# Kernel optimization log

Hardware: AMD Instinct MI355X
Metric: run time of the kernel (lower is better)

Reference implementation:

```python
import jax, jax.numpy as jnp
import numpy as np

DIM = 2048
N_HEADS = 16
HEAD_DIM = DIM // N_HEADS
ROPE_DIMS = 16
SEQ_LEN = 512
BATCH = 16


def _rope_cache(T):
    # freqs: [T, rd/2]
    inv = 1.0 / (10000.0 ** (jnp.arange(0, ROPE_DIMS, 2, dtype=jnp.float32) / ROPE_DIMS))
    t = jnp.arange(T, dtype=jnp.float32)
    freqs = jnp.outer(t, inv)
    return jnp.cos(freqs), jnp.sin(freqs)


def _apply_rope(x, cos, sin):
    # x: [B, H, T, hd]; rotate first ROPE_DIMS dims (half-split style)
    rd = ROPE_DIMS
    x_rope, x_pass = x[..., :rd], x[..., rd:]
    x1, x2 = x_rope[..., : rd // 2], x_rope[..., rd // 2:]
    c = cos[None, None, :, :]
    s = sin[None, None, :, :]
    rot = jnp.concatenate([x1 * c - x2 * s, x2 * c + x1 * s], axis=-1)
    return jnp.concatenate([rot, x_pass], axis=-1)


def setup_inputs() -> dict:
    key = jax.random.key(0)
    k1, k2, k3 = jax.random.split(key, 3)
    x = jax.random.normal(k1, (BATCH, SEQ_LEN, DIM), dtype=jnp.float32)
    Wqkv = jax.random.normal(k2, (DIM, 3 * DIM), dtype=jnp.float32) * (1.0 / np.sqrt(DIM))
    Wout = jax.random.normal(k3, (DIM, DIM), dtype=jnp.float32) * (1.0 / np.sqrt(DIM))
    return {"x": x, "Wqkv": Wqkv, "Wout": Wout}


def reference(x, Wqkv, Wout):
    B, T, C = x.shape
    H, hd = N_HEADS, HEAD_DIM
    qkv = (x @ Wqkv).reshape(B, T, 3, H, hd)
    q, k, v = qkv[:, :, 0], qkv[:, :, 1], qkv[:, :, 2]  # [B, T, H, hd]
    q = jnp.transpose(q, (0, 2, 1, 3))  # [B, H, T, hd]
    k = jnp.transpose(k, (0, 2, 1, 3))
    v = jnp.transpose(v, (0, 2, 1, 3))
    cos, sin = _rope_cache(T)
    q = _apply_rope(q, cos, sin)
    k = _apply_rope(k, cos, sin)
    scale = 1.0 / np.sqrt(hd)
    scores = jnp.einsum('bhqd,bhkd->bhqk', q, k) * scale
    causal = jnp.tril(jnp.ones((T, T), dtype=bool))
    scores = jnp.where(causal[None, None], scores, jnp.finfo(scores.dtype).min)
    attn = jax.nn.softmax(scores, axis=-1)
    y = jnp.einsum('bhqk,bhkd->bhqd', attn, v)  # [B, H, T, hd]
    y = jnp.transpose(y, (0, 2, 1, 3)).reshape(B, T, C)
    return y @ Wout
```

## Files before the change

### kernel.cpp

```cpp
#include <hip/hip_runtime.h>
#include <hip/hip_bf16.h>
#include <math.h>

using bf16 = __hip_bfloat16;
typedef short s16x8 __attribute__((ext_vector_type(8)));
typedef short s16x4 __attribute__((ext_vector_type(4)));
typedef float f32x4 __attribute__((ext_vector_type(4)));

#define DIM_C   2048
#define NHEADS  16
#define HEADD   128
#define SEQT    512
#define NBATCH  16
#define MROWS   (NBATCH*SEQT)
#define QKVN    (3*DIM_C)

static __device__ __forceinline__ float bf2f(bf16 v){ return __bfloat162float(v); }

static __device__ __forceinline__ void gl16(const void* g, void* l){
    __builtin_amdgcn_global_load_lds(
        reinterpret_cast<__attribute__((address_space(1))) void*>(
            (unsigned long long)g),
        reinterpret_cast<__attribute__((address_space(3))) void*>(
            (unsigned long long)l),
        16, 0, 0);
}

__global__ void k_cvt(const float* __restrict__ in, bf16* __restrict__ out, int n){
    size_t i = ((size_t)blockIdx.x*blockDim.x + threadIdx.x)*8;
    if (i >= (size_t)n) return;
    float4 a = *(const float4*)(in+i);
    float4 b = *(const float4*)(in+i+4);
    union { bf16 o[8]; s16x8 v; } u;
    u.o[0]=__float2bfloat16(a.x); u.o[1]=__float2bfloat16(a.y);
    u.o[2]=__float2bfloat16(a.z); u.o[3]=__float2bfloat16(a.w);
    u.o[4]=__float2bfloat16(b.x); u.o[5]=__float2bfloat16(b.y);
    u.o[6]=__float2bfloat16(b.z); u.o[7]=__float2bfloat16(b.w);
    *(s16x8*)(out+i) = u.v;
}

__global__ void k_transpose_cvt(const float* __restrict__ in, bf16* __restrict__ out,
                                int R, int C){
    __shared__ float tile[32][33];
    int c0 = blockIdx.x*32, r0 = blockIdx.y*32;
    int tx = threadIdx.x, ty = threadIdx.y;
    #pragma unroll
    for(int i=0;i<4;i++)
        tile[ty+8*i][tx] = in[(size_t)(r0+ty+8*i)*C + c0+tx];
    __syncthreads();
    #pragma unroll
    for(int i=0;i<4;i++)
        out[(size_t)(c0+ty+8*i)*R + r0+tx] = __float2bfloat16(tile[tx][ty+8*i]);
}

__global__ void k_vtrans(const bf16* __restrict__ qkv, bf16* __restrict__ vt){
    __shared__ bf16 tile[32][33];
    int t0 = blockIdx.x*32, d0 = blockIdx.y*32, bh = blockIdx.z;
    int b = bh>>4, h = bh&15;
    int tx = threadIdx.x, ty = threadIdx.y;
    const bf16* src = qkv + ((size_t)b*SEQT)*QKVN + 2*DIM_C + (size_t)h*HEADD;
    #pragma unroll
    for(int i=0;i<4;i++)
        tile[ty+8*i][tx] = src[(size_t)(t0+ty+8*i)*QKVN + d0+tx];
    __syncthreads();
    bf16* dst = vt + ((size_t)bh*HEADD)*SEQT;
    #pragma unroll
    for(int i=0;i<4;i++)
        dst[(size_t)(d0+ty+8*i)*SEQT + t0+tx] = tile[tx][ty+8*i];
}

__global__ void k_rope(bf16* __restrict__ qkv){
    int tid = blockIdx.x*blockDim.x + threadIdx.x;
    int i   = tid & 7;        int rest = tid >> 3;
    int qk  = rest & 1;       rest >>= 1;
    int h   = rest & 15;      rest >>= 4;
    int t   = rest & 511;     int b = rest >> 9;
    size_t base = ((size_t)(b*SEQT + t))*QKVN + (size_t)qk*DIM_C + (size_t)h*HEADD;
    float x1 = bf2f(qkv[base+i]), x2 = bf2f(qkv[base+i+8]);
    float inv = powf(10000.f, -(float)i/8.f);
    float fr = (float)t * inv;
    float c = cosf(fr), s = sinf(fr);
    qkv[base+i]   = __float2bfloat16(x1*c - x2*s);
    qkv[base+i+8] = __float2bfloat16(x2*c + x1*s);
}

static __device__ __forceinline__ void store_c(bf16* p, float v){ *p = __float2bfloat16(v); }
static __device__ __forceinline__ void store_c(float* p, float v){ *p = v; }

#define BAR()   __builtin_amdgcn_s_barrier()
#define SCHED() __builtin_amdgcn_sched_barrier(0)
#define LGKM0() asm volatile("s_waitcnt lgkmcnt(0)" ::: "memory")
#define VM6()   asm volatile("s_waitcnt vmcnt(6)"   ::: "memory")
#define VM0()   asm volatile("s_waitcnt vmcnt(0)"   ::: "memory")

template<typename OutT>
__global__ __launch_bounds__(512, 2) void k_gemm256(const bf16* __restrict__ A,
                                                    const bf16* __restrict__ Bt,
                                                    OutT* __restrict__ C,
                                                    int M, int N, int K){
    __shared__ __align__(16) bf16 AS[2][2][128*64];
    __shared__ __align__(16) bf16 BS[2][2][128*64];
    const int tid = threadIdx.x;
    const int wave = tid>>6, lane = tid&63, quad = lane>>4, l16 = lane&15;
    const int wm = wave>>2, wn = wave&3;

    const int nbx = gridDim.x;
    const int nwg = gridDim.x*gridDim.y;
    int bid = blockIdx.y*nbx + blockIdx.x;
    int swz = (bid&7)*(nwg>>3) + (bid>>3);
    int by = swz / nbx, bx = swz - by*nbx;
    const size_t rowbase = (size_t)by * 256;
    const size_t colbase = (size_t)bx * 256;
    const int NT = K>>6;

    f32x4 acc[8][4];
    #pragma unroll
    for(int i=0;i<8;i++)
        #pragma unroll
        for(int j=0;j<4;j++) acc[i][j] = (f32x4)(0.f);

    int cb0 = wave*64,        cc0 = cb0 + lane;
    int cb1 = 512 + wave*64,  cc1 = cb1 + lane;
    int ri0 = cc0>>3, gg0 = (cc0&7)^(ri0&7);
    int ri1 = cc1>>3, gg1 = (cc1&7)^(ri1&7);
    const bf16* pA0[2];  const bf16* pA1[2];
    const bf16* pB0[2];  const bf16* pB1[2];
    pA0[0] = A  + (rowbase + (size_t)(((ri0>>6)<<7) + (ri0&63)))*(size_t)K + gg0*8;
    pA0[1] = A  + (rowbase + (size_t)(((ri1>>6)<<7) + (ri1&63)))*(size_t)K + gg1*8;
    pA1[0] = pA0[0] + (size_t)64*K;  pA1[1] = pA0[1] + (size_t)64*K;
    pB0[0] = Bt + (colbase + (size_t)(((ri0>>5)<<6) + (ri0&31)))*(size_t)K + gg0*8;
    pB0[1] = Bt + (colbase + (size_t)(((ri1>>5)<<6) + (ri1&31)))*(size_t)K + gg1*8;
    pB1[0] = pB0[0] + (size_t)32*K;  pB1[1] = pB0[1] + (size_t)32*K;
    const int dE0 = cb0*8, dE1 = cb1*8;

    const int x7 = l16 & 7;
    int aB[2], bB[2];
    #pragma unroll
    for(int kc=0;kc<2;kc++){
        int ch = ((kc*4+quad) ^ x7) << 3;
        aB[kc] = (wm*64 + l16)*64 + ch;
        bB[kc] = (wn*32 + l16)*64 + ch;
    }

    s16x8 af[4][2], bf0[2][2], bf1[2][2];

#define READ_AF(BUF,MH) do{ _Pragma("unroll")                                    \
    for(int kc_=0;kc_<2;kc_++){ _Pragma("unroll")                                \
        for(int mi_=0;mi_<4;mi_++)                                               \
            af[mi_][kc_] = *(const s16x8*)(&AS[BUF][MH][aB[kc_] + mi_*1024]); } }while(0)
#define READ_BF(BUF,NH,DST) do{ _Pragma("unroll")                                \
    for(int kc_=0;kc_<2;kc_++){ _Pragma("unroll")                                \
        for(int nj_=0;nj_<2;nj_++)                                               \
            DST[nj_][kc_] = *(const s16x8*)(&BS[BUF][NH][bB[kc_] + nj_*1024]); } }while(0)
#define MFMA16(BFR,MH,NH) do{ _Pragma("unroll")                                  \
    for(int kc_=0;kc_<2;kc_++){ _Pragma("unroll")                                \
        for(int mi_=0;mi_<4;mi_++){ _Pragma("unroll")                            \
            for(int nj_=0;nj_<2;nj_++)                                           \
                acc[(MH)*4+mi_][(NH)*2+nj_] =                                    \
                    __builtin_amdgcn_mfma_f32_16x16x32_bf16(                     \
                        af[mi_][kc_], BFR[nj_][kc_],                             \
                        acc[(MH)*4+mi_][(NH)*2+nj_], 0,0,0); } } }while(0)

#define STG_A0(BUF,OFF) do{ gl16(pA0[0]+(OFF), &AS[BUF][0][dE0]);                \
                            gl16(pA0[1]+(OFF), &AS[BUF][0][dE1]); }while(0)
#define STG_A1(BUF,OFF) do{ gl16(pA1[0]+(OFF), &AS[BUF][1][dE0]);                \
                            gl16(pA1[1]+(OFF), &AS[BUF][1][dE1]); }while(0)
#define STG_B0(BUF,OFF) do{ gl16(pB0[0]+(OFF), &BS[BUF][0][dE0]);                \
                            gl16(pB0[1]+(OFF), &BS[BUF][0][dE1]); }while(0)
#define STG_B1(BUF,OFF) do{ gl16(pB1[0]+(OFF), &BS[BUF][1][dE0]);                \
                            gl16(pB1[1]+(OFF), &BS[BUF][1][dE1]); }while(0)

#define TILE(BUF,O1,O2,GA1,GR)                                                   \
    do{                                                                          \
                                                                         \
        if (GA1) STG_A1(BUF^1, O1);                                              \
        READ_AF(BUF,0); READ_BF(BUF,0,bf0);                                      \
        BAR(); LGKM0(); SCHED();                                                 \
        __builtin_amdgcn_s_setprio(1);  MFMA16(bf0,0,0);                         \
        __builtin_amdgcn_s_setprio(0);                                           \
        BAR(); SCHED();                                                          \
                                                                         \
        if (GR) STG_A0(BUF,O2);                                                  \
        READ_BF(BUF,1,bf1);                                                      \
        BAR(); LGKM0(); SCHED();                                                 \
        __builtin_amdgcn_s_setprio(1);  MFMA16(bf1,0,1);                         \
        __builtin_amdgcn_s_setprio(0);                                           \
        BAR(); SCHED();                                                          \
                                                                         \
        if (GR) STG_B0(BUF,O2);                                                  \
        READ_AF(BUF,1);                                                          \
        BAR(); LGKM0(); SCHED();                                                 \
        __builtin_amdgcn_s_setprio(1);  MFMA16(bf0,1,0);                         \
        __builtin_amdgcn_s_setprio(0);                                           \
        BAR(); SCHED();                                                          \
                                                                         \
        if (GR){ STG_B1(BUF,O2); VM6(); } else { VM0(); }                        \
        BAR(); SCHED();                                                          \
        __builtin_amdgcn_s_setprio(1);  MFMA16(bf1,1,1);                         \
        __builtin_amdgcn_s_setprio(0);                                           \
        BAR(); SCHED();                                                          \
    }while(0)

    STG_A0(0,0); STG_B0(0,0); STG_B1(0,0); STG_A1(0,0);
    STG_A0(1,64); STG_B0(1,64); STG_B1(1,64);
    VM6();
    BAR(); SCHED();

    for(int g=0; g<NT; g+=2){
        const bool p2 = (g+2 < NT), p3 = (g+3 < NT);
        TILE(0, 64, 128, true, p2);
        TILE(1, 128, 192, p2, p3);
        pA0[0]+=128; pA0[1]+=128; pA1[0]+=128; pA1[1]+=128;
        pB0[0]+=128; pB0[1]+=128; pB1[0]+=128; pB1[1]+=128;
    }
#undef TILE
#undef STG_A0
#undef STG_A1
#undef STG_B0
#undef STG_B1
#undef MFMA16
#undef READ_BF
#undef READ_AF

    #pragma unroll
    for(int mf=0;mf<8;mf++)
        #pragma unroll
        for(int nf=0;nf<4;nf++)
            #pragma unroll
            for(int r=0;r<4;r++){
                size_t row = rowbase + wm*128 + mf*16 + quad*4 + r;
                size_t col = colbase + wn*64  + nf*16 + l16;
                store_c(C + row*(size_t)N + col, acc[mf][nf][r]);
            }
}

__global__ __launch_bounds__(256, 4) void k_attn(const bf16* __restrict__ qkv,
                                                 const bf16* __restrict__ vt,
                                                 bf16* __restrict__ y){
    __shared__ __align__(16) bf16 Ks[64*128];
    __shared__ __align__(16) bf16 Vs[128*64];
    __shared__ __align__(16) bf16 Ps[64*64];
    const int id = blockIdx.x;
    const int x  = id & 7, g = id >> 3;
    const int qt = 7 - (g >> 5);
    const int bh = ((g & 31) << 3) | x;
    const int b = bh >> 4, h = bh & 15;
    const int tid = threadIdx.x, wave = tid>>6, lane = tid&63, quad = lane>>4, l16 = lane&15;
    const int qbase = qt*64;
    const size_t rs = QKVN;
    const bf16* Qg = qkv + ((size_t)b*SEQT)*rs + (size_t)h*HEADD;
    const bf16* Kg = Qg + DIM_C;
    const bf16* Vtbh = vt + ((size_t)bh*HEADD)*SEQT;

    s16x8 qf[4];
    const int qrow = qbase + wave*16 + l16;
    {
        #pragma unroll
        for(int kc=0;kc<4;kc++)
            qf[kc] = *(const s16x8*)(Qg + (size_t)qrow*rs + kc*32 + quad*8);
    }
    f32x4 acc_o[8];
    #pragma unroll
    for(int dt=0;dt<8;dt++) acc_o[dt] = (f32x4)(0.f);
    float lsum = 0.f;
    const float C2 = 0.12751745f;
    const int nkt = qt + 1;

    for(int kt=0; kt<nkt; kt++){
        const int kbase = kt*64;
        const bool diag = (kt == nkt-1);
        __syncthreads();
        #pragma unroll
        for(int i=0;i<4;i++){
            int base = wave*256 + i*64;
            int cc   = base + lane;
            int rk   = cc>>4, gk = (cc&15) ^ (rk&7);
            gl16(Kg + (size_t)(kbase+rk)*rs + gk*8, &Ks[base*8]);
            int rv   = cc>>3, gv = (cc&7) ^ (rv&7);
            gl16(Vtbh + (size_t)rv*SEQT + kbase + gv*8, &Vs[base*8]);
        }
        __syncthreads();
        f32x4 sacc[4];
        #pragma unroll
        for(int ni=0;ni<4;ni++) sacc[ni] = (f32x4)(0.f);
        #pragma unroll
        for(int kc=0;kc<4;kc++){
            const int ch = kc*4 + quad;
            #pragma unroll
            for(int ni=0;ni<4;ni++){
                int r = ni*16 + l16;
                s16x8 kf = *(const s16x8*)(&Ks[r*128 + ((ch ^ (r&7))*8)]);
                sacc[ni] = __builtin_amdgcn_mfma_f32_16x16x32_bf16(kf, qf[kc], sacc[ni], 0,0,0);
            }
        }
        {
            const int row = wave*16 + l16;
            const int r7  = row & 7;
            #pragma unroll
            for(int ni=0;ni<4;ni++){
                union { s16x4 v; bf16 hh[4]; } pk;
                #pragma unroll
                for(int rr=0;rr<4;rr++){
                    float e = exp2f(sacc[ni][rr]*C2);
                    if (diag){ int kcol = kbase + ni*16 + quad*4 + rr; if (kcol > qrow) e = 0.f; }
                    lsum += e;
                    pk.hh[rr] = __float2bfloat16(e);
                }
                int c = ni*2 + (quad>>1);
                *(s16x4*)(&Ps[row*64 + ((c ^ r7)<<3) + ((quad&1)<<2)]) = pk.v;
            }
        }
        #pragma unroll
        for(int kk=0;kk<2;kk++){
            int rw = wave*16 + l16;
            int c  = kk*4 + quad;
            s16x8 pf = *(const s16x8*)(&Ps[rw*64 + ((c ^ (rw&7))<<3)]);
            #pragma unroll
            for(int dt=0;dt<8;dt++){
                int r = dt*16 + l16;
                s16x8 vf = *(const s16x8*)(&Vs[r*64 + ((c ^ (r&7))<<3)]);
                acc_o[dt] = __builtin_amdgcn_mfma_f32_16x16x32_bf16(vf, pf, acc_o[dt], 0,0,0);
            }
        }
    }
    lsum += __shfl_xor(lsum, 16, 64);
    lsum += __shfl_xor(lsum, 32, 64);
    float inv_l = 1.f/lsum;
    size_t base = ((size_t)(b*SEQT) + qrow)*DIM_C + (size_t)h*HEADD;
    #pragma unroll
    for(int dt=0;dt<8;dt++){
        union { s16x4 v; bf16 hh[4]; } o;
        #pragma unroll
        for(int rr=0;rr<4;rr++) o.hh[rr] = __float2bfloat16(acc_o[dt][rr]*inv_l);
        *(s16x4*)(y + base + dt*16 + quad*4) = o.v;
    }
}

extern "C" void kernel_launch(void* const* d_in, const int* in_sizes, int n_in,
                              void* d_out, int out_size, void* d_ws, size_t ws_size,
                              hipStream_t stream){
    const float* x    = (const float*)d_in[0];
    const float* Wqkv = (const float*)d_in[1];
    const float* Wout = (const float*)d_in[2];
    float* out = (float*)d_out;
    char* ws = (char*)d_ws;
    bf16* xb    = (bf16*)(ws + 0);
    bf16* vt    = (bf16*)(ws + 0);
    bf16* wqkvT = (bf16*)(ws + 33554432);
    bf16* woutT = (bf16*)(ws + 58720256);
    bf16* qkv   = (bf16*)(ws + 67108864);
    bf16* yb    = (bf16*)(ws + 167772160);

    k_cvt<<<dim3(MROWS*DIM_C/8/256), 256, 0, stream>>>(x, xb, MROWS*DIM_C);
    dim3 tb(32,8);
    k_transpose_cvt<<<dim3(QKVN/32, DIM_C/32), tb, 0, stream>>>(Wqkv, wqkvT, DIM_C, QKVN);
    k_transpose_cvt<<<dim3(DIM_C/32, DIM_C/32), tb, 0, stream>>>(Wout, woutT, DIM_C, DIM_C);

    k_gemm256<bf16><<<dim3(QKVN/256, MROWS/256), 512, 0, stream>>>(xb, wqkvT, qkv, MROWS, QKVN, DIM_C);
    k_rope<<<dim3(NBATCH*SEQT*NHEADS*2*8/256), 256, 0, stream>>>(qkv);
    k_vtrans<<<dim3(SEQT/32, HEADD/32, NBATCH*NHEADS), tb, 0, stream>>>(qkv, vt);
    k_attn<<<dim3(SEQT/64 * NHEADS * NBATCH), 256, 0, stream>>>(qkv, vt, yb);
    k_gemm256<float><<<dim3(DIM_C/256, MROWS/256), 512, 0, stream>>>(yb, woutT, out, MROWS, DIM_C, DIM_C);
}
```

Measured before the change: 492.3 us.

## Fuse RoPE and V transpose into QKV GEMM epilogue

The QKV projection GEMM now applies RoPE to Q/K columns in its epilogue, using a lane shuffle to pair rotated halves. It also writes V directly in the transposed per-head layout, so the separate rope and vtrans kernels and their extra global memory passes are removed. The QK output is stored with a narrower row stride and V goes to its own buffer. The costs are per-element trig in the epilogue and scattered 8-byte V stores.

New measurement: 509.7 us. 1.04x slower.

```diff
diff --git a/kernel.cpp b/kernel.cpp
--- a/kernel.cpp
+++ b/kernel.cpp
@@ -14,6 +14,7 @@
 #define NBATCH  16
 #define MROWS   (NBATCH*SEQT)
 #define QKVN    (3*DIM_C)
+#define QKN     (2*DIM_C)
 
 static __device__ __forceinline__ float bf2f(bf16 v){ return __bfloat162float(v); }
 
@@ -53,37 +54,6 @@
         out[(size_t)(c0+ty+8*i)*R + r0+tx] = __float2bfloat16(tile[tx][ty+8*i]);
 }
 
-__global__ void k_vtrans(const bf16* __restrict__ qkv, bf16* __restrict__ vt){
-    __shared__ bf16 tile[32][33];
-    int t0 = blockIdx.x*32, d0 = blockIdx.y*32, bh = blockIdx.z;
-    int b = bh>>4, h = bh&15;
-    int tx = threadIdx.x, ty = threadIdx.y;
-    const bf16* src = qkv + ((size_t)b*SEQT)*QKVN + 2*DIM_C + (size_t)h*HEADD;
-    #pragma unroll
-    for(int i=0;i<4;i++)
-        tile[ty+8*i][tx] = src[(size_t)(t0+ty+8*i)*QKVN + d0+tx];
-    __syncthreads();
-    bf16* dst = vt + ((size_t)bh*HEADD)*SEQT;
-    #pragma unroll
-    for(int i=0;i<4;i++)
-        dst[(size_t)(d0+ty+8*i)*SEQT + t0+tx] = tile[tx][ty+8*i];
-}
-
-__global__ void k_rope(bf16* __restrict__ qkv){
-    int tid = blockIdx.x*blockDim.x + threadIdx.x;
-    int i   = tid & 7;        int rest = tid >> 3;
-    int qk  = rest & 1;       rest >>= 1;
-    int h   = rest & 15;      rest >>= 4;
-    int t   = rest & 511;     int b = rest >> 9;
-    size_t base = ((size_t)(b*SEQT + t))*QKVN + (size_t)qk*DIM_C + (size_t)h*HEADD;
-    float x1 = bf2f(qkv[base+i]), x2 = bf2f(qkv[base+i+8]);
-    float inv = powf(10000.f, -(float)i/8.f);
-    float fr = (float)t * inv;
-    float c = cosf(fr), s = sinf(fr);
-    qkv[base+i]   = __float2bfloat16(x1*c - x2*s);
-    qkv[base+i+8] = __float2bfloat16(x2*c + x1*s);
-}
-
 static __device__ __forceinline__ void store_c(bf16* p, float v){ *p = __float2bfloat16(v); }
 static __device__ __forceinline__ void store_c(float* p, float v){ *p = v; }
 
@@ -93,10 +63,11 @@
 #define VM6()   asm volatile("s_waitcnt vmcnt(6)"   ::: "memory")
 #define VM0()   asm volatile("s_waitcnt vmcnt(0)"   ::: "memory")
 
-template<typename OutT>
+template<typename OutT, int MODE>
 __global__ __launch_bounds__(512, 2) void k_gemm256(const bf16* __restrict__ A,
                                                     const bf16* __restrict__ Bt,
                                                     OutT* __restrict__ C,
+                                                    bf16* __restrict__ vt,
                                                     int M, int N, int K){
     __shared__ __align__(16) bf16 AS[2][2][128*64];
     __shared__ __align__(16) bf16 BS[2][2][128*64];
@@ -222,19 +193,59 @@
 #undef READ_BF
 #undef READ_AF
 
-    #pragma unroll
-    for(int mf=0;mf<8;mf++)
-        #pragma unroll
-        for(int nf=0;nf<4;nf++)
-            #pragma unroll
-            for(int r=0;r<4;r++){
-                size_t row = rowbase + wm*128 + mf*16 + quad*4 + r;
-                size_t col = colbase + wn*64  + nf*16 + l16;
-                store_c(C + row*(size_t)N + col, acc[mf][nf][r]);
+    if (MODE == 0){
+        #pragma unroll
+        for(int mf=0;mf<8;mf++)
+            #pragma unroll
+            for(int nf=0;nf<4;nf++)
+                #pragma unroll
+                for(int r=0;r<4;r++){
+                    size_t row = rowbase + wm*128 + mf*16 + quad*4 + r;
+                    size_t col = colbase + wn*64  + nf*16 + l16;
+                    store_c(C + row*(size_t)N + col, acc[mf][nf][r]);
+                }
+    } else if (colbase < 4096){
+        const bool ropeW = ((wn&1) == 0);
+        const float inv = powf(10000.f, -(float)(l16&7)/8.f);
+        const bool hi = (l16 >= 8);
+        #pragma unroll
+        for(int mf=0;mf<8;mf++)
+            #pragma unroll
+            for(int nf=0;nf<4;nf++)
+                #pragma unroll
+                for(int r=0;r<4;r++){
+                    size_t row = rowbase + wm*128 + mf*16 + quad*4 + r;
+                    size_t col = colbase + wn*64  + nf*16 + l16;
+                    float val = acc[mf][nf][r];
+                    if (nf == 0 && ropeW){
+                        int t = (int)(row & 511);
+                        float fr = (float)t * inv;
+                        float cc = cosf(fr), ss = sinf(fr);
+                        float p  = __shfl_xor(val, 8, 64);
+                        val = hi ? (val*cc + p*ss) : (val*cc - p*ss);
+                    }
+                    *( (bf16*)C + row*(size_t)QKN + col ) = __float2bfloat16(val);
+                }
+    } else {
+        #pragma unroll
+        for(int nf=0;nf<4;nf++){
+            int col = (int)colbase + wn*64 + nf*16 + l16;
+            int h   = (col - 4096) >> 7;
+            int d   = col & 127;
+            #pragma unroll
+            for(int mf=0;mf<8;mf++){
+                int row0 = (int)rowbase + wm*128 + mf*16 + quad*4;
+                int b = row0 >> 9, t0 = row0 & 511;
+                union { s16x4 v; bf16 hh[4]; } o;
+                #pragma unroll
+                for(int r=0;r<4;r++) o.hh[r] = __float2bfloat16(acc[mf][nf][r]);
+                *(s16x4*)(vt + ((size_t)((b<<4)+h)*128 + d)*512 + t0) = o.v;
             }
-}
-
-__global__ __launch_bounds__(256, 4) void k_attn(const bf16* __restrict__ qkv,
+        }
+    }
+}
+
+__global__ __launch_bounds__(256, 4) void k_attn(const bf16* __restrict__ qk,
                                                  const bf16* __restrict__ vt,
                                                  bf16* __restrict__ y){
     __shared__ __align__(16) bf16 Ks[64*128];
@@ -247,8 +258,8 @@
     const int b = bh >> 4, h = bh & 15;
     const int tid = threadIdx.x, wave = tid>>6, lane = tid&63, quad = lane>>4, l16 = lane&15;
     const int qbase = qt*64;
-    const size_t rs = QKVN;
-    const bf16* Qg = qkv + ((size_t)b*SEQT)*rs + (size_t)h*HEADD;
+    const size_t rs = QKN;
+    const bf16* Qg = qk + ((size_t)b*SEQT)*rs + (size_t)h*HEADD;
     const bf16* Kg = Qg + DIM_C;
     const bf16* Vtbh = vt + ((size_t)bh*HEADD)*SEQT;
 
@@ -345,10 +356,10 @@
     float* out = (float*)d_out;
     char* ws = (char*)d_ws;
     bf16* xb    = (bf16*)(ws + 0);
-    bf16* vt    = (bf16*)(ws + 0);
     bf16* wqkvT = (bf16*)(ws + 33554432);
     bf16* woutT = (bf16*)(ws + 58720256);
-    bf16* qkv   = (bf16*)(ws + 67108864);
+    bf16* qkb   = (bf16*)(ws + 67108864);
+    bf16* vt    = (bf16*)(ws + 134217728);
     bf16* yb    = (bf16*)(ws + 167772160);
 
     k_cvt<<<dim3(MROWS*DIM_C/8/256), 256, 0, stream>>>(x, xb, MROWS*DIM_C);
@@ -356,9 +367,9 @@
     k_transpose_cvt<<<dim3(QKVN/32, DIM_C/32), tb, 0, stream>>>(Wqkv, wqkvT, DIM_C, QKVN);
     k_transpose_cvt<<<dim3(DIM_C/32, DIM_C/32), tb, 0, stream>>>(Wout, woutT, DIM_C, DIM_C);
 
-    k_gemm256<bf16><<<dim3(QKVN/256, MROWS/256), 512, 0, stream>>>(xb, wqkvT, qkv, MROWS, QKVN, DIM_C);
-    k_rope<<<dim3(NBATCH*SEQT*NHEADS*2*8/256), 256, 0, stream>>>(qkv);
-    k_vtrans<<<dim3(SEQT/32, HEADD/32, NBATCH*NHEADS), tb, 0, stream>>>(qkv, vt);
-    k_attn<<<dim3(SEQT/64 * NHEADS * NBATCH), 256, 0, stream>>>(qkv, vt, yb);
-    k_gemm256<float><<<dim3(DIM_C/256, MROWS/256), 512, 0, stream>>>(yb, woutT, out, MROWS, DIM_C, DIM_C);
-}
+    k_gemm256<bf16,1><<<dim3(QKVN/256, MROWS/256), 512, 0, stream>>>(
+        xb, wqkvT, qkb, vt, MROWS, QKVN, DIM_C);
+    k_attn<<<dim3(SEQT/64 * NHEADS * NBATCH), 256, 0, stream>>>(qkb, vt, yb);
+    k_gemm256<float,0><<<dim3(DIM_C/256, MROWS/256), 512, 0, stream>>>(
+        yb, woutT, out, (bf16*)nullptr, MROWS, DIM_C, DIM_C);
+}
```
